# Kernel tuning notes

Hardware: AMD Instinct MI355X
Metric: run time of the kernel (lower is better)

## Reference

```python
import jax, jax.numpy as jnp
import numpy as np
import math

B, CK, CV, H, W = 16, 64, 512, 56, 56


def setup_inputs() -> dict:
    key = jax.random.key(0)
    k1, k2, k3, k4 = jax.random.split(key, 4)
    return {
        "mk": jax.random.normal(k1, (B, CK, H, W), dtype=jnp.float32),
        "qk": jax.random.normal(k2, (B, CK, H, W), dtype=jnp.float32),
        "mv": jax.random.normal(k3, (B, CV, H, W), dtype=jnp.float32),
        "qv": jax.random.normal(k4, (B, CV, H, W), dtype=jnp.float32),
    }


def reference(mk, qk, mv, qv):
    b, ck, h, w = qk.shape
    cv = mv.shape[1]
    n = h * w
    qk_f = qk.reshape(b, ck, n)          # [B, CK, HW] query keys
    mk_f = mk.reshape(b, ck, -1)         # [B, CK, N_mem]
    # squared-L2 affinity (query-norm term is constant per column -> dropped, cancels in softmax)
    a = jnp.sum(mk_f * mk_f, axis=1)[:, :, None]                # [B, N_mem, 1]
    bb = 2.0 * jnp.einsum('bcn,bcm->bnm', mk_f, qk_f)           # [B, N_mem, HW]
    affinity = (-a + bb) / math.sqrt(ck)
    affinity = jax.nn.softmax(affinity, axis=1)                 # softmax over memory dim
    # readout: weighted sum of memory values
    mem = jnp.einsum('bcn,bnm->bcm', mv.reshape(b, cv, -1), affinity)
    mem = mem.reshape(b, cv, h, w)
    return mem, qv
```

## Files before the change

### kernel.cpp

```cpp
#include <hip/hip_runtime.h>


#define B_   16
#define CK_  64
#define CV_  512
#define N_   3136
#define NPAD 3200
#define TM   64
#define TN   128
#define NITER 25
#define NBLK32 100
#define NBLK16 200

typedef __bf16 bf16_t;
typedef bf16_t bf16x8 __attribute__((ext_vector_type(8)));
typedef bf16_t bf16x4 __attribute__((ext_vector_type(4)));
typedef float  f32x16 __attribute__((ext_vector_type(16)));
typedef float  f32x4  __attribute__((ext_vector_type(4)));
typedef float  float4_t __attribute__((ext_vector_type(4)));

#define SCALE_DOT 0.36067376022224085f

__global__ __launch_bounds__(256) void prep_kq(const float* __restrict__ mk,
                                               const float* __restrict__ qk,
                                               bf16_t* __restrict__ Kf,
                                               bf16_t* __restrict__ Qf,
                                               float* __restrict__ a2) {
  int idx = blockIdx.x * 256 + threadIdx.x;
  int b = idx / NPAD, n = idx % NPAD;
  bool valid = n < N_;
  int l32n = n & 31, nblk = n >> 5;
  float ss = 0.f;
  const float* mkp = mk + (size_t)b * CK_ * N_ + n;
  const float* qkp = qk + (size_t)b * CK_ * N_ + n;
  bf16x8* Kf8 = (bf16x8*)Kf;
  bf16x8* Qf8 = (bf16x8*)Qf;
  #pragma unroll
  for (int cc = 0; cc < 8; cc++) {
    bf16x8 kv, qv8;
    #pragma unroll
    for (int j = 0; j < 8; j++) {
      int c = 8 * cc + j;
      float kx = valid ? mkp[(size_t)c * N_] : 0.f;
      float qx = valid ? qkp[(size_t)c * N_] : 0.f;
      ss += kx * kx;
      kv[j] = (bf16_t)kx;
      qv8[j] = (bf16_t)qx;
    }
    int s = cc >> 1, hh = cc & 1;
    size_t pos = (((size_t)b * NBLK32 + nblk) * 4 + s) * 64 + l32n + 32 * hh;
    Kf8[pos] = kv;
    Qf8[pos] = qv8;
  }
  a2[idx] = valid ? ss * 0.5f : 3.0e38f;
}

#define VCHUNK 512
__global__ __launch_bounds__(256) void prep_v(const float* __restrict__ mv,
                                              bf16_t* __restrict__ Vf) {
  __shared__ __align__(16) bf16_t T[32][VCHUNK];
  int wg = blockIdx.x;
  int chunk = wg % 7;
  int t2 = wg / 7;
  int cblk = t2 & 15;
  int b = t2 >> 4;
  int n0 = chunk * VCHUNK;
  int tid = threadIdx.x;

  const float* base = mv + ((size_t)b * CV_ + cblk * 32) * N_;
  #pragma unroll
  for (int rep = 0; rep < 16; rep++) {
    int idx = rep * 256 + tid;
    int cl = idx >> 7;
    int np = (idx & 127) * 4;
    int n = n0 + np;
    bf16x4 o;
    if (n < N_) {
      f32x4 v = *(const f32x4*)(base + (size_t)cl * N_ + n);
      #pragma unroll
      for (int j = 0; j < 4; j++) o[j] = (bf16_t)v[j];
    } else {
      #pragma unroll
      for (int j = 0; j < 4; j++) o[j] = (bf16_t)0.f;
    }
    *(bf16x4*)((char*)T + cl * (VCHUNK * 2) + ((np * 2) ^ ((cl & 7) << 4))) = o;
  }
  __syncthreads();

  bf16x8* Vf8 = (bf16x8*)Vf;
  size_t outbase = (((size_t)b * 16 + cblk) * NBLK16 + (n0 >> 4)) * 64;
  #pragma unroll
  for (int pass = 0; pass < 8; pass++) {
    int idx = pass * 256 + tid;
    int nb = idx >> 6;
    int ln = idx & 63;
    if (n0 + nb * 16 < NPAD) {
      int cl = ln & 31;
      int n_loc = nb * 16 + (ln >> 5) * 8;
      bf16x8 o = *(bf16x8*)((char*)T + cl * (VCHUNK * 2) +
                            ((n_loc * 2) ^ ((cl & 7) << 4)));
      Vf8[outbase + (size_t)nb * 64 + ln] = o;
    }
  }
}

__global__ __launch_bounds__(256) void copy_qv(const float4_t* __restrict__ src,
                                               float4_t* __restrict__ dst) {
  size_t i = (size_t)blockIdx.x * 256 + threadIdx.x;
  dst[i] = src[i];
}

__global__ __launch_bounds__(512, 2) void attn_main(const bf16_t* __restrict__ Kf,
                                                    const bf16_t* __restrict__ Qf,
                                                    const float* __restrict__ A2S,
                                                    const bf16_t* __restrict__ Vf,
                                                    float* __restrict__ out) {
  const int xcd = blockIdx.x & 7;
  const int idx = blockIdx.x >> 3;
  const int q49 = idx / 49;
  const int b   = xcd * 2 + q49;
  const int m0  = (idx - q49 * 49) * TM;

  const int tid  = threadIdx.x;
  const int w    = tid >> 6;
  const int lane = tid & 63;
  const int l32  = lane & 31;
  const int h    = lane >> 5;
  const int g    = w >> 2;
  const int i    = w & 3;

  __shared__ __align__(16) bf16_t Plds[2][64][128];
  __shared__ float  Llds[8][32];
  __shared__ float  Linv[64];

  const bf16x8* Qf8 = (const bf16x8*)Qf;
  const int mblk = (m0 >> 5) + g;
  bf16x8 qfrag[4];
  #pragma unroll
  for (int s = 0; s < 4; s++)
    qfrag[s] = Qf8[(((size_t)b * NBLK32 + mblk) * 4 + s) * 64 + lane];

  f32x16 acc[2][2];
  #pragma unroll
  for (int cb = 0; cb < 2; cb++)
    #pragma unroll
    for (int mb = 0; mb < 2; mb++)
      #pragma unroll
      for (int r = 0; r < 16; r++) acc[cb][mb][r] = 0.f;

  float Lpart = 0.f;
  const float*  a2b = A2S + (size_t)b * NPAD;
  const bf16x8* Kf8 = (const bf16x8*)Kf;
  const bf16x8* Vf8 = (const bf16x8*)Vf + (((size_t)b * 16 + 2 * w) * NBLK16) * 64 + lane;

  const int wrow = 32 * g + l32;
  const int wswz = (wrow & 15) << 4;
  const int rswz = (l32 & 15) << 4;

  for (int iter = 0; iter < NITER; iter++) {
    const int n0 = iter * TN + 32 * i;

    const bf16x8* kp = Kf8 + (((size_t)b * NBLK32 + (iter * 4 + i)) * 4) * 64 + lane;
    bf16x8 kf0 = kp[0], kf1 = kp[64], kf2 = kp[128], kf3 = kp[192];
    f32x4 na[4];
    #pragma unroll
    for (int t = 0; t < 4; t++)
      na[t] = *(const f32x4*)(a2b + n0 + 8 * t + 4 * h);
    const bf16x8* vp = Vf8 + (size_t)iter * 8 * 64;
    bf16x8 vf[16];
    #pragma unroll
    for (int t = 0; t < 8; t++) {
      vf[2 * t]     = vp[t * 64];
      vf[2 * t + 1] = vp[t * 64 + NBLK16 * 64];
    }

    f32x16 sacc;
    #pragma unroll
    for (int t = 0; t < 4; t++)
      #pragma unroll
      for (int q = 0; q < 4; q++) sacc[4 * t + q] = -na[t][q];
    sacc = __builtin_amdgcn_mfma_f32_32x32x16_bf16(kf0, qfrag[0], sacc, 0, 0, 0);
    sacc = __builtin_amdgcn_mfma_f32_32x32x16_bf16(kf1, qfrag[1], sacc, 0, 0, 0);
    sacc = __builtin_amdgcn_mfma_f32_32x32x16_bf16(kf2, qfrag[2], sacc, 0, 0, 0);
    sacc = __builtin_amdgcn_mfma_f32_32x32x16_bf16(kf3, qfrag[3], sacc, 0, 0, 0);

    char* Pb = (char*)Plds[iter & 1];
    #pragma unroll
    for (int t = 0; t < 4; t++) {
      bf16x4 pk;
      #pragma unroll
      for (int q = 0; q < 4; q++) {
        float p = __builtin_amdgcn_exp2f(sacc[4 * t + q] * SCALE_DOT);
        Lpart += p;
        pk[q] = (bf16_t)p;
      }
      int colb = 64 * i + 16 * t + 8 * h;
      *(bf16x4*)(Pb + wrow * 256 + (colb ^ wswz)) = pk;
    }

    asm volatile("s_waitcnt lgkmcnt(0)" ::: "memory");
    __builtin_amdgcn_s_barrier();

    #pragma unroll
    for (int t = 0; t < 8; t++) {
      bf16x8 pf0 = *(const bf16x8*)(Pb + l32 * 256 + ((32 * t + 16 * h) ^ rswz));
      bf16x8 pf1 = *(const bf16x8*)(Pb + (32 + l32) * 256 + ((32 * t + 16 * h) ^ rswz));
      acc[0][0] = __builtin_amdgcn_mfma_f32_32x32x16_bf16(vf[2 * t],     pf0, acc[0][0], 0, 0, 0);
      acc[0][1] = __builtin_amdgcn_mfma_f32_32x32x16_bf16(vf[2 * t],     pf1, acc[0][1], 0, 0, 0);
      acc[1][0] = __builtin_amdgcn_mfma_f32_32x32x16_bf16(vf[2 * t + 1], pf0, acc[1][0], 0, 0, 0);
      acc[1][1] = __builtin_amdgcn_mfma_f32_32x32x16_bf16(vf[2 * t + 1], pf1, acc[1][1], 0, 0, 0);
    }
  }

  Lpart += __shfl_xor(Lpart, 32, 64);
  if (h == 0) Llds[w][l32] = Lpart;
  __syncthreads();
  if (tid < 64) {
    int gg = tid >> 5;
    float s = 0.f;
    #pragma unroll
    for (int ww = 0; ww < 4; ww++) s += Llds[4 * gg + ww][tid & 31];
    Linv[tid] = 1.0f / s;
  }
  __syncthreads();

  #pragma unroll
  for (int cb = 0; cb < 2; cb++) {
    #pragma unroll
    for (int mb = 0; mb < 2; mb++) {
      float rl = Linv[32 * mb + l32];
      #pragma unroll
      for (int reg = 0; reg < 16; reg++) {
        int r = (reg & 3) + 8 * (reg >> 2) + 4 * h;
        int c = 64 * w + 32 * cb + r;
        out[((size_t)b * CV_ + c) * N_ + m0 + 32 * mb + l32] = acc[cb][mb][reg] * rl;
      }
    }
  }
}

extern "C" void kernel_launch(void* const* d_in, const int* in_sizes, int n_in,
                              void* d_out, int out_size, void* d_ws, size_t ws_size,
                              hipStream_t stream) {
  const float* mk = (const float*)d_in[0];
  const float* qk = (const float*)d_in[1];
  const float* mv = (const float*)d_in[2];
  const float* qv = (const float*)d_in[3];
  float* out = (float*)d_out;

  char* ws = (char*)d_ws;
  bf16_t* Kf = (bf16_t*)(ws);
  bf16_t* Qf = (bf16_t*)(ws + 6553600);
  float*  a2 = (float*)(ws + 13107200);
  bf16_t* Vf = (bf16_t*)(ws + 13312000);

  prep_kq<<<dim3((B_ * NPAD) / 256), dim3(256), 0, stream>>>(mk, qk, Kf, Qf, a2);
  prep_v<<<dim3(B_ * 16 * 7), dim3(256), 0, stream>>>(mv, Vf);
  attn_main<<<dim3(B_ * 49), dim3(512), 0, stream>>>(Kf, Qf, a2, Vf, out);
  copy_qv<<<dim3((B_ * CV_ * N_) / 4 / 256), dim3(256), 0, stream>>>(
      (const float4_t*)qv, (float4_t*)(out + (size_t)B_ * CV_ * N_));
}
```

Measured before the change: 636.7 us.

## Double query tile per block and fuse qv copy into attention main loop

Doubles the query tile from 64 to 128 columns, so each workgroup reuses every loaded K and V fragment across four 32-column query blocks instead of two. This halves global K/V traffic per output and cuts the grid from 784 to 400 blocks. The separate qv copy kernel is removed, and the copy is interleaved into the first 16 iterations of the attention loop so it overlaps with compute. The V fragment load is split into two halves around the barrier to limit register pressure. Risks are higher register use under the 2-waves occupancy bound, a padded last tile that now needs output masking, and fewer blocks for the available CUs.

```diff
diff --git a/kernel.cpp b/kernel.cpp
--- a/kernel.cpp
+++ b/kernel.cpp
@@ -6,7 +6,7 @@
 #define CV_  512
 #define N_   3136
 #define NPAD 3200
-#define TM   64
+#define TM   128
 #define TN   128
 #define NITER 25
 #define NBLK32 100
@@ -17,7 +17,6 @@
 typedef bf16_t bf16x4 __attribute__((ext_vector_type(4)));
 typedef float  f32x16 __attribute__((ext_vector_type(16)));
 typedef float  f32x4  __attribute__((ext_vector_type(4)));
-typedef float  float4_t __attribute__((ext_vector_type(4)));
 
 #define SCALE_DOT 0.36067376022224085f
 
@@ -104,22 +103,17 @@
   }
 }
 
-__global__ __launch_bounds__(256) void copy_qv(const float4_t* __restrict__ src,
-                                               float4_t* __restrict__ dst) {
-  size_t i = (size_t)blockIdx.x * 256 + threadIdx.x;
-  dst[i] = src[i];
-}
-
 __global__ __launch_bounds__(512, 2) void attn_main(const bf16_t* __restrict__ Kf,
                                                     const bf16_t* __restrict__ Qf,
                                                     const float* __restrict__ A2S,
                                                     const bf16_t* __restrict__ Vf,
+                                                    const float* __restrict__ qv,
                                                     float* __restrict__ out) {
   const int xcd = blockIdx.x & 7;
   const int idx = blockIdx.x >> 3;
-  const int q49 = idx / 49;
-  const int b   = xcd * 2 + q49;
-  const int m0  = (idx - q49 * 49) * TM;
+  const int q25 = idx / 25;
+  const int b   = xcd * 2 + q25;
+  const int m0  = (idx - q25 * 25) * TM;
 
   const int tid  = threadIdx.x;
   const int w    = tid >> 6;
@@ -129,36 +123,45 @@
   const int g    = w >> 2;
   const int i    = w & 3;
 
-  __shared__ __align__(16) bf16_t Plds[2][64][128];
-  __shared__ float  Llds[8][32];
-  __shared__ float  Linv[64];
+  __shared__ __align__(16) char pool[65536];
 
   const bf16x8* Qf8 = (const bf16x8*)Qf;
-  const int mblk = (m0 >> 5) + g;
-  bf16x8 qfrag[4];
-  #pragma unroll
-  for (int s = 0; s < 4; s++)
-    qfrag[s] = Qf8[(((size_t)b * NBLK32 + mblk) * 4 + s) * 64 + lane];
-
-  f32x16 acc[2][2];
+  bf16x8 qfrag[2][4];
+  #pragma unroll
+  for (int jj = 0; jj < 2; jj++)
+    #pragma unroll
+    for (int s = 0; s < 4; s++)
+      qfrag[jj][s] = Qf8[(((size_t)b * NBLK32 + (m0 >> 5) + 2 * g + jj) * 4 + s) * 64 + lane];
+
+  f32x16 acc[2][4];
   #pragma unroll
   for (int cb = 0; cb < 2; cb++)
     #pragma unroll
-    for (int mb = 0; mb < 2; mb++)
+    for (int mb = 0; mb < 4; mb++)
       #pragma unroll
       for (int r = 0; r < 16; r++) acc[cb][mb][r] = 0.f;
 
-  float Lpart = 0.f;
+  float Lp[2] = {0.f, 0.f};
   const float*  a2b = A2S + (size_t)b * NPAD;
   const bf16x8* Kf8 = (const bf16x8*)Kf;
   const bf16x8* Vf8 = (const bf16x8*)Vf + (((size_t)b * 16 + 2 * w) * NBLK16) * 64 + lane;
 
-  const int wrow = 32 * g + l32;
-  const int wswz = (wrow & 15) << 4;
   const int rswz = (l32 & 15) << 4;
+
+  const f32x4* qsrc = (const f32x4*)qv;
+  f32x4* qdst = (f32x4*)(out + (size_t)B_ * CV_ * N_);
+  const size_t QT = (size_t)B_ * CV_ * N_ / 4;
+  const size_t qbase = (size_t)blockIdx.x * 16384;
+  f32x4 qr0, qr1;
 
   for (int iter = 0; iter < NITER; iter++) {
     const int n0 = iter * TN + 32 * i;
+
+    if (iter >= 1 && iter <= 16) {
+      size_t qi = qbase + (size_t)(iter - 1) * 1024 + tid;
+      if (qi < QT) qdst[qi] = qr0;
+      if (qi + 512 < QT) qdst[qi + 512] = qr1;
+    }
 
     const bf16x8* kp = Kf8 + (((size_t)b * NBLK32 + (iter * 4 + i)) * 4) * 64 + lane;
     bf16x8 kf0 = kp[0], kf1 = kp[64], kf2 = kp[128], kf3 = kp[192];
@@ -167,59 +170,86 @@
     for (int t = 0; t < 4; t++)
       na[t] = *(const f32x4*)(a2b + n0 + 8 * t + 4 * h);
     const bf16x8* vp = Vf8 + (size_t)iter * 8 * 64;
-    bf16x8 vf[16];
-    #pragma unroll
-    for (int t = 0; t < 8; t++) {
-      vf[2 * t]     = vp[t * 64];
-      vf[2 * t + 1] = vp[t * 64 + NBLK16 * 64];
-    }
-
-    f32x16 sacc;
-    #pragma unroll
-    for (int t = 0; t < 4; t++)
-      #pragma unroll
-      for (int q = 0; q < 4; q++) sacc[4 * t + q] = -na[t][q];
-    sacc = __builtin_amdgcn_mfma_f32_32x32x16_bf16(kf0, qfrag[0], sacc, 0, 0, 0);
-    sacc = __builtin_amdgcn_mfma_f32_32x32x16_bf16(kf1, qfrag[1], sacc, 0, 0, 0);
-    sacc = __builtin_amdgcn_mfma_f32_32x32x16_bf16(kf2, qfrag[2], sacc, 0, 0, 0);
-    sacc = __builtin_amdgcn_mfma_f32_32x32x16_bf16(kf3, qfrag[3], sacc, 0, 0, 0);
-
-    char* Pb = (char*)Plds[iter & 1];
+    bf16x8 vfA[8];
     #pragma unroll
     for (int t = 0; t < 4; t++) {
-      bf16x4 pk;
-      #pragma unroll
-      for (int q = 0; q < 4; q++) {
-        float p = __builtin_amdgcn_exp2f(sacc[4 * t + q] * SCALE_DOT);
-        Lpart += p;
-        pk[q] = (bf16_t)p;
+      vfA[2 * t]     = vp[t * 64];
+      vfA[2 * t + 1] = vp[t * 64 + NBLK16 * 64];
+    }
+    if (iter < 16) {
+      size_t qi = qbase + (size_t)iter * 1024 + tid;
+      if (qi < QT) qr0 = qsrc[qi];
+      if (qi + 512 < QT) qr1 = qsrc[qi + 512];
+    }
+
+    char* Pb = pool + (iter & 1) * 32768;
+    #pragma unroll
+    for (int jj = 0; jj < 2; jj++) {
+      f32x16 sacc;
+      #pragma unroll
+      for (int t = 0; t < 4; t++)
+        #pragma unroll
+        for (int q = 0; q < 4; q++) sacc[4 * t + q] = -na[t][q];
+      sacc = __builtin_amdgcn_mfma_f32_32x32x16_bf16(kf0, qfrag[jj][0], sacc, 0, 0, 0);
+      sacc = __builtin_amdgcn_mfma_f32_32x32x16_bf16(kf1, qfrag[jj][1], sacc, 0, 0, 0);
+      sacc = __builtin_amdgcn_mfma_f32_32x32x16_bf16(kf2, qfrag[jj][2], sacc, 0, 0, 0);
+      sacc = __builtin_amdgcn_mfma_f32_32x32x16_bf16(kf3, qfrag[jj][3], sacc, 0, 0, 0);
+
+      const int wrow = 32 * (2 * g + jj) + l32;
+      const int wswz = (l32 & 15) << 4;
+      #pragma unroll
+      for (int t = 0; t < 4; t++) {
+        bf16x4 pk;
+        #pragma unroll
+        for (int q = 0; q < 4; q++) {
+          float p = __builtin_amdgcn_exp2f(sacc[4 * t + q] * SCALE_DOT);
+          Lp[jj] += p;
+          pk[q] = (bf16_t)p;
+        }
+        int colb = 64 * i + 16 * t + 8 * h;
+        *(bf16x4*)(Pb + wrow * 256 + (colb ^ wswz)) = pk;
       }
-      int colb = 64 * i + 16 * t + 8 * h;
-      *(bf16x4*)(Pb + wrow * 256 + (colb ^ wswz)) = pk;
     }
 
     asm volatile("s_waitcnt lgkmcnt(0)" ::: "memory");
     __builtin_amdgcn_s_barrier();
 
+    bf16x8 vfB[8];
+    #pragma unroll
+    for (int t = 0; t < 4; t++) {
+      vfB[2 * t]     = vp[(t + 4) * 64];
+      vfB[2 * t + 1] = vp[(t + 4) * 64 + NBLK16 * 64];
+    }
+
     #pragma unroll
     for (int t = 0; t < 8; t++) {
-      bf16x8 pf0 = *(const bf16x8*)(Pb + l32 * 256 + ((32 * t + 16 * h) ^ rswz));
-      bf16x8 pf1 = *(const bf16x8*)(Pb + (32 + l32) * 256 + ((32 * t + 16 * h) ^ rswz));
-      acc[0][0] = __builtin_amdgcn_mfma_f32_32x32x16_bf16(vf[2 * t],     pf0, acc[0][0], 0, 0, 0);
-      acc[0][1] = __builtin_amdgcn_mfma_f32_32x32x16_bf16(vf[2 * t],     pf1, acc[0][1], 0, 0, 0);
-      acc[1][0] = __builtin_amdgcn_mfma_f32_32x32x16_bf16(vf[2 * t + 1], pf0, acc[1][0], 0, 0, 0);
-      acc[1][1] = __builtin_amdgcn_mfma_f32_32x32x16_bf16(vf[2 * t + 1], pf1, acc[1][1], 0, 0, 0);
-    }
-  }
-
-  Lpart += __shfl_xor(Lpart, 32, 64);
-  if (h == 0) Llds[w][l32] = Lpart;
-  __syncthreads();
-  if (tid < 64) {
-    int gg = tid >> 5;
+      bf16x8 va0 = (t < 4) ? vfA[2 * t]     : vfB[2 * (t - 4)];
+      bf16x8 va1 = (t < 4) ? vfA[2 * t + 1] : vfB[2 * (t - 4) + 1];
+      #pragma unroll
+      for (int mb = 0; mb < 4; mb++) {
+        bf16x8 pf = *(const bf16x8*)(Pb + (32 * mb + l32) * 256 + ((32 * t + 16 * h) ^ rswz));
+        acc[0][mb] = __builtin_amdgcn_mfma_f32_32x32x16_bf16(va0, pf, acc[0][mb], 0, 0, 0);
+        acc[1][mb] = __builtin_amdgcn_mfma_f32_32x32x16_bf16(va1, pf, acc[1][mb], 0, 0, 0);
+      }
+    }
+  }
+
+  __syncthreads();
+  Lp[0] += __shfl_xor(Lp[0], 32, 64);
+  Lp[1] += __shfl_xor(Lp[1], 32, 64);
+  float* Llds = (float*)pool;
+  float* Linv = (float*)(pool + 2048);
+  if (h == 0) {
+    Llds[(w * 2 + 0) * 32 + l32] = Lp[0];
+    Llds[(w * 2 + 1) * 32 + l32] = Lp[1];
+  }
+  __syncthreads();
+  if (tid < 128) {
+    int mb = tid >> 5, l = tid & 31;
+    int g2 = mb >> 1, jj = mb & 1;
     float s = 0.f;
     #pragma unroll
-    for (int ww = 0; ww < 4; ww++) s += Llds[4 * gg + ww][tid & 31];
+    for (int ww = 0; ww < 4; ww++) s += Llds[((4 * g2 + ww) * 2 + jj) * 32 + l];
     Linv[tid] = 1.0f / s;
   }
   __syncthreads();
@@ -227,13 +257,16 @@
   #pragma unroll
   for (int cb = 0; cb < 2; cb++) {
     #pragma unroll
-    for (int mb = 0; mb < 2; mb++) {
-      float rl = Linv[32 * mb + l32];
-      #pragma unroll
-      for (int reg = 0; reg < 16; reg++) {
-        int r = (reg & 3) + 8 * (reg >> 2) + 4 * h;
-        int c = 64 * w + 32 * cb + r;
-        out[((size_t)b * CV_ + c) * N_ + m0 + 32 * mb + l32] = acc[cb][mb][reg] * rl;
+    for (int mb = 0; mb < 4; mb++) {
+      int m = m0 + 32 * mb + l32;
+      if (m < N_) {
+        float rl = Linv[32 * mb + l32];
+        #pragma unroll
+        for (int reg = 0; reg < 16; reg++) {
+          int r = (reg & 3) + 8 * (reg >> 2) + 4 * h;
+          int c = 64 * w + 32 * cb + r;
+          out[((size_t)b * CV_ + c) * N_ + m] = acc[cb][mb][reg] * rl;
+        }
       }
     }
   }
@@ -256,7 +289,5 @@
 
   prep_kq<<<dim3((B_ * NPAD) / 256), dim3(256), 0, stream>>>(mk, qk, Kf, Qf, a2);
   prep_v<<<dim3(B_ * 16 * 7), dim3(256), 0, stream>>>(mv, Vf);
-  attn_main<<<dim3(B_ * 49), dim3(512), 0, stream>>>(Kf, Qf, a2, Vf, out);
-  copy_qv<<<dim3((B_ * CV_ * N_) / 4 / 256), dim3(256), 0, stream>>>(
-      (const float4_t*)qv, (float4_t*)(out + (size_t)B_ * CV_ * N_));
-}
+  attn_main<<<dim3(B_ * 25), dim3(512), 0, stream>>>(Kf, Qf, a2, Vf, qv, out);
+}
```

Result: slower. 725.6 us (+14.0%).
